# Performance work log

Hardware: AMD Instinct MI355X
Metric: run time of the kernel (lower is better)

## Reference

```python
import jax, jax.numpy as jnp
import numpy as np

NUM_EMBEDDINGS = 2048
EMBEDDING_DIM = 256
COMMITMENT_COST = 0.25


def setup_inputs() -> dict:
    key = jax.random.key(0)
    k1, k2 = jax.random.split(key)
    inputs = jax.random.normal(k1, (2, EMBEDDING_DIM, 24, 24, 24), dtype=jnp.float32)
    embedding_weight = jax.random.normal(k2, (NUM_EMBEDDINGS, EMBEDDING_DIM), dtype=jnp.float32)
    return {"inputs": inputs, "embedding_weight": embedding_weight}


def reference(inputs, embedding_weight):
    # [B, C, D, H, W] -> [B, D, H, W, C]
    x = jnp.transpose(inputs, (0, 2, 3, 4, 1))
    in_shape = x.shape
    flat = x.reshape(-1, EMBEDDING_DIM)  # [N, D]

    distances = (
        jnp.sum(flat * flat, axis=1, keepdims=True)
        + jnp.sum(embedding_weight * embedding_weight, axis=1)
        - 2.0 * flat @ embedding_weight.T
    )
    encoding_indices = jnp.argmin(distances, axis=1)  # [N]
    encodings = jax.nn.one_hot(encoding_indices, NUM_EMBEDDINGS, dtype=jnp.float32)  # [N, K]

    # Gather instead of one_hot @ W (same math, no redundant GEMM)
    quantized = embedding_weight[encoding_indices].reshape(in_shape)

    e_latent_loss = jnp.mean((jax.lax.stop_gradient(quantized) - x) ** 2)
    loss = COMMITMENT_COST * e_latent_loss

    # Straight-through estimator
    quantized_st = x + jax.lax.stop_gradient(quantized - x)

    avg_probs = jnp.mean(encodings, axis=0)
    perplexity = jnp.exp(-jnp.sum(avg_probs * jnp.log(avg_probs + 1e-10)))

    quantized_out = jnp.transpose(quantized_st, (0, 4, 1, 2, 3))
    return (loss, quantized_out, perplexity, encodings, encoding_indices[:, None])
```

## Files before the change

kernel.cpp:

```cpp
#include <hip/hip_runtime.h>

#define S_SP   13824
#define CHAN   256
#define NQ     27648
#define KCODES 2048
#define CS     3538944
#define OFF_Q   1
#define OFF_PPL 7077889
#define OFF_ENC 7077890LL
#define OFF_IDX 63700994LL

typedef __bf16 bf16x8 __attribute__((ext_vector_type(8)));
typedef float  f32x4  __attribute__((ext_vector_type(4)));

#define GLOAD_LDS16(g, s)                                                      \
  __builtin_amdgcn_global_load_lds(                                            \
      (const __attribute__((address_space(1))) void*)(g),                      \
      (__attribute__((address_space(3))) void*)(s), 16, 0, 0)

__device__ __forceinline__ unsigned int f2bf(float f) {
  unsigned int u = __float_as_uint(f);
  unsigned int r = u + 0x7FFFu + ((u >> 16) & 1u);
  return r >> 16;
}
__device__ __forceinline__ float bf2f(unsigned int h) {
  return __uint_as_float(h << 16);
}
__device__ __forceinline__ void fsplit(float f, unsigned int& hi, unsigned int& lo) {
  hi = f2bf(f);
  float r = f - bf2f(hi);
  lo = f2bf(r);
}

__global__ __launch_bounds__(256) void prep_w(const float* __restrict__ W,
                                              unsigned short* __restrict__ Wh,
                                              unsigned short* __restrict__ Wl,
                                              float* __restrict__ wn) {
  int g = blockIdx.x * 256 + threadIdx.x;
  int row = g >> 5;
  int d0 = (g & 31) * 8;
  const float* Wp = W + (size_t)row * CHAN + d0;
  float v[8];
  *(float4*)(v) = *(const float4*)Wp;
  *(float4*)(v + 4) = *(const float4*)(Wp + 4);
  float s = 0.f;
  unsigned int h[8], l[8];
#pragma unroll
  for (int j = 0; j < 8; ++j) {
    s = fmaf(v[j], v[j], s);
    fsplit(v[j], h[j], l[j]);
  }
  int4 ph, pl;
  ph.x = (int)(h[0] | (h[1] << 16)); ph.y = (int)(h[2] | (h[3] << 16));
  ph.z = (int)(h[4] | (h[5] << 16)); ph.w = (int)(h[6] | (h[7] << 16));
  pl.x = (int)(l[0] | (l[1] << 16)); pl.y = (int)(l[2] | (l[3] << 16));
  pl.z = (int)(l[4] | (l[5] << 16)); pl.w = (int)(l[6] | (l[7] << 16));
  *(int4*)(Wh + (size_t)row * CHAN + d0) = ph;
  *(int4*)(Wl + (size_t)row * CHAN + d0) = pl;
  for (int off = 16; off; off >>= 1) s += __shfl_down(s, off);
  if ((threadIdx.x & 31) == 0) wn[row] = s;
}

__global__ __launch_bounds__(256) void prep_x(const float* __restrict__ X,
                                              unsigned short* __restrict__ Xh,
                                              unsigned short* __restrict__ Xl) {
  __shared__ float xs[32 * 257];
  int t = threadIdx.x;
  int qb = blockIdx.x * 32;
  int b = qb / S_SP, s0 = qb % S_SP;
  const float* xp = X + (size_t)b * CS + s0;
  int q = t & 31;
  int db = t >> 5;
  for (int r = 0; r < 32; ++r) {
    int d = db + (r << 3);
    xs[q * 257 + d] = xp[(size_t)d * S_SP + q];
  }
  __syncthreads();
  int row = t >> 3, c8 = t & 7;
  size_t obase = (size_t)(qb + row) * CHAN;
  const float* rp0 = xs + row * 257;
#pragma unroll
  for (int j = 0; j < 4; ++j) {
    int d = j * 64 + c8 * 8;
    const float* rp = rp0 + d;
    unsigned int h[8], l[8];
#pragma unroll
    for (int e = 0; e < 8; ++e) fsplit(rp[e], h[e], l[e]);
    int4 ph, pl;
    ph.x = (int)(h[0] | (h[1] << 16)); ph.y = (int)(h[2] | (h[3] << 16));
    ph.z = (int)(h[4] | (h[5] << 16)); ph.w = (int)(h[6] | (h[7] << 16));
    pl.x = (int)(l[0] | (l[1] << 16)); pl.y = (int)(l[2] | (l[3] << 16));
    pl.z = (int)(l[4] | (l[5] << 16)); pl.w = (int)(l[6] | (l[7] << 16));
    *(int4*)(Xh + obase + d) = ph;
    *(int4*)(Xl + obase + d) = pl;
  }
}

__global__ __launch_bounds__(256, 2) void dist_mfma(const unsigned short* __restrict__ Xh,
                                                    const unsigned short* __restrict__ Xl,
                                                    const unsigned short* __restrict__ Wh,
                                                    const unsigned short* __restrict__ Wl,
                                                    const float* __restrict__ wn,
                                                    float* __restrict__ rB1,
                                                    int* __restrict__ rI1,
                                                    float* __restrict__ rB2) {
  __shared__ __align__(16) unsigned short sW[2][2][4096];
  __shared__ float wnl[1024];
  int t = threadIdx.x;
  int w = t >> 6, l = t & 63;
  int lr = l & 15, lc = l >> 4;
  int kg = blockIdx.x & 1;
  int qb = (blockIdx.x >> 1) * 128;
  int kofs = kg << 10;

  for (int j = t; j < 1024; j += 256) wnl[j] = wn[kofs + j];

  bf16x8 ah[2][8], al[2][8];
#pragma unroll
  for (int s = 0; s < 2; ++s) {
    size_t base = (size_t)(qb + w * 32 + s * 16 + lr) * CHAN + lc * 8;
#pragma unroll
    for (int c = 0; c < 8; ++c) {
      ah[s][c] = *(const bf16x8*)(Xh + base + c * 32);
      al[s][c] = *(const bf16x8*)(Xl + base + c * 32);
    }
  }

  float b1[2][4], b2[2][4]; int i1[2][4];
#pragma unroll
  for (int s = 0; s < 2; ++s)
#pragma unroll
    for (int r = 0; r < 4; ++r) { b1[s][r] = 3.4e38f; b2[s][r] = 3.4e38f; i1[s][r] = 0; }

  auto stage = [&](int buf, int kt) {
    size_t rb = (size_t)(kofs + (kt << 4) + lr) * CHAN + lc * 8;
    GLOAD_LDS16(Wh + rb + w * 32,        &sW[buf][0][w * 512]);
    GLOAD_LDS16(Wh + rb + (w + 4) * 32,  &sW[buf][0][(w + 4) * 512]);
    GLOAD_LDS16(Wl + rb + w * 32,        &sW[buf][1][w * 512]);
    GLOAD_LDS16(Wl + rb + (w + 4) * 32,  &sW[buf][1][(w + 4) * 512]);
  };

  stage(0, 0);
  __syncthreads();

  for (int kt = 0; kt < 64; ++kt) {
    int cur = kt & 1;
    if (kt < 63) stage(cur ^ 1, kt + 1);
    f32x4 a0 = {0.f, 0.f, 0.f, 0.f}, a1 = {0.f, 0.f, 0.f, 0.f};
#pragma unroll
    for (int c = 0; c < 8; ++c) {
      bf16x8 bh = *(const bf16x8*)&sW[cur][0][c * 512 + (l << 3)];
      bf16x8 bl = *(const bf16x8*)&sW[cur][1][c * 512 + (l << 3)];
      a0 = __builtin_amdgcn_mfma_f32_16x16x32_bf16(ah[0][c], bh, a0, 0, 0, 0);
      a1 = __builtin_amdgcn_mfma_f32_16x16x32_bf16(ah[1][c], bh, a1, 0, 0, 0);
      a0 = __builtin_amdgcn_mfma_f32_16x16x32_bf16(al[0][c], bh, a0, 0, 0, 0);
      a1 = __builtin_amdgcn_mfma_f32_16x16x32_bf16(al[1][c], bh, a1, 0, 0, 0);
      a0 = __builtin_amdgcn_mfma_f32_16x16x32_bf16(ah[0][c], bl, a0, 0, 0, 0);
      a1 = __builtin_amdgcn_mfma_f32_16x16x32_bf16(ah[1][c], bl, a1, 0, 0, 0);
    }
    int k = kofs + (kt << 4) + lr;
    float wnk = wnl[(kt << 4) + lr];
#pragma unroll
    for (int r = 0; r < 4; ++r) {
      float s0 = fmaf(-2.0f, a0[r], wnk);
      bool lt0 = s0 < b1[0][r];
      b2[0][r] = fminf(b2[0][r], fmaxf(s0, b1[0][r]));
      b1[0][r] = lt0 ? s0 : b1[0][r];
      i1[0][r] = lt0 ? k : i1[0][r];
      float s1 = fmaf(-2.0f, a1[r], wnk);
      bool lt1 = s1 < b1[1][r];
      b2[1][r] = fminf(b2[1][r], fmaxf(s1, b1[1][r]));
      b1[1][r] = lt1 ? s1 : b1[1][r];
      i1[1][r] = lt1 ? k : i1[1][r];
    }
    __syncthreads();
  }

#pragma unroll
  for (int m = 1; m < 16; m <<= 1) {
#pragma unroll
    for (int s = 0; s < 2; ++s)
#pragma unroll
      for (int r = 0; r < 4; ++r) {
        float ob1 = __shfl_xor(b1[s][r], m);
        int   oi  = __shfl_xor(i1[s][r], m);
        float ob2 = __shfl_xor(b2[s][r], m);
        bool sw = (ob1 < b1[s][r]) || (ob1 == b1[s][r] && oi < i1[s][r]);
        b2[s][r] = fminf(fmaxf(b1[s][r], ob1), fminf(b2[s][r], ob2));
        b1[s][r] = sw ? ob1 : b1[s][r];
        i1[s][r] = sw ? oi : i1[s][r];
      }
  }
  if (lr == 0) {
#pragma unroll
    for (int s = 0; s < 2; ++s)
#pragma unroll
      for (int r = 0; r < 4; ++r) {
        int q = qb + w * 32 + s * 16 + lc * 4 + r;
        size_t o = (size_t)kg * NQ + q;
        rB1[o] = b1[s][r]; rI1[o] = i1[s][r]; rB2[o] = b2[s][r];
      }
  }
}

__global__ __launch_bounds__(256) void merge_emit(const float* __restrict__ rB1,
                                                  const int* __restrict__ rI1,
                                                  const float* __restrict__ rB2,
                                                  float* __restrict__ outF,
                                                  int* __restrict__ flagcount,
                                                  int2* __restrict__ flaglist) {
  int t = threadIdx.x;
  int r = t >> 5, j = t & 31;
  int n = blockIdx.x * 8 + r;

  float B1 = rB1[n]; int I1 = rI1[n]; float B2 = rB2[n];
  float c1 = rB1[NQ + n]; int ci = rI1[NQ + n]; float c2 = rB2[NQ + n];
  bool sw = (c1 < B1) || (c1 == B1 && ci < I1);
  float nb2 = fminf(fmaxf(B1, c1), fminf(B2, c2));
  float nb1 = sw ? c1 : B1;
  int   ni  = sw ? ci : I1;

  if (j == 0) {
    if (nb2 - nb1 < 0.05f) {
      int slot = atomicAdd(flagcount, 1);
      flaglist[slot] = make_int2(n, ni);
    }
    outF[OFF_IDX + n] = (float)ni;
  }

  float* row = outF + OFF_ENC + (size_t)n * KCODES;
#pragma unroll
  for (int k = 0; k < 32; ++k) {
    int col = 2 * j + 64 * k;
    union { float f[2]; unsigned long long u; } v;
    v.f[0] = (col == ni) ? 1.0f : 0.0f;
    v.f[1] = (col + 1 == ni) ? 1.0f : 0.0f;
    __builtin_nontemporal_store(v.u, (unsigned long long*)(row + col));
  }
}

__global__ __launch_bounds__(256) void refine2(const float* __restrict__ X,
                                               const float* __restrict__ W,
                                               const int* __restrict__ flagcount,
                                               const int2* __restrict__ flaglist,
                                               float* __restrict__ outF) {
  __shared__ double xd[CHAN];
  __shared__ double rv[256];
  __shared__ int    ri[256];
  int t = threadIdx.x;
  int cnt = flagcount[0];
  for (int jj = blockIdx.x; jj < cnt; jj += gridDim.x) {
    __syncthreads();
    int2 e = flaglist[jj];
    int n = e.x, prov = e.y;
    int b = n / S_SP, s = n % S_SP;
    xd[t] = (double)X[(size_t)b * CS + (size_t)t * S_SP + s];
    __syncthreads();

    double best = 1e300;
    int bi = 1 << 30;
    for (int j8 = 0; j8 < 8; ++j8) {
      int k = t * 8 + j8;
      const float* Wp = W + (size_t)k * CHAN;
      double dsum = 0.0;
      for (int d = 0; d < CHAN; ++d) {
        double df = xd[d] - (double)Wp[d];
        dsum = fma(df, df, dsum);
      }
      if (dsum < best) { best = dsum; bi = k; }
    }
    rv[t] = best; ri[t] = bi;
    __syncthreads();
    for (int off = 128; off > 0; off >>= 1) {
      if (t < off) {
        if (rv[t + off] < rv[t] || (rv[t + off] == rv[t] && ri[t + off] < ri[t])) {
          rv[t] = rv[t + off]; ri[t] = ri[t + off];
        }
      }
      __syncthreads();
    }
    if (t == 0) {
      int fin = ri[0];
      outF[OFF_IDX + n] = (float)fin;
      if (fin != prov) {
        float* row = outF + OFF_ENC + (size_t)n * KCODES;
        row[prov] = 0.0f;
        row[fin]  = 1.0f;
      }
    }
  }
}

__global__ __launch_bounds__(256) void scatter_stats(const float* __restrict__ X,
                                                     const float* __restrict__ W,
                                                     float* __restrict__ outF,
                                                     int* __restrict__ counts,
                                                     float* __restrict__ loss_acc) {
  __shared__ int sidx[64];
  __shared__ float wred[4];
  int t = threadIdx.x;
  int q = t & 63, cg = t >> 6;
  int n = blockIdx.x * 64 + q;
  if (t < 64) {
    int idx = (int)outF[OFF_IDX + n];
    sidx[t] = idx;
    atomicAdd(&counts[idx], 1);
  }
  __syncthreads();
  int idx = sidx[q];
  int b = n / S_SP, s = n % S_SP;
  const float* Wp = W + (size_t)idx * CHAN;
  const float* xp = X + (size_t)b * CS + s;
  float* qp = outF + OFF_Q + (size_t)b * CS + s;

  float lsum = 0.f;
#pragma unroll 8
  for (int k = 0; k < 64; ++k) {
    int c = cg + (k << 2);
    float wv = Wp[c];
    float xv = xp[(size_t)c * S_SP];
    qp[(size_t)c * S_SP] = wv;
    float df = wv - xv;
    lsum = fmaf(df, df, lsum);
  }

  for (int off = 32; off; off >>= 1) lsum += __shfl_down(lsum, off);
  if ((t & 63) == 0) wred[t >> 6] = lsum;
  __syncthreads();
  if (t == 0) atomicAdd(loss_acc, wred[0] + wred[1] + wred[2] + wred[3]);
}

__global__ __launch_bounds__(256) void finalize(const int* __restrict__ counts,
                                                const float* __restrict__ loss_acc,
                                                float* __restrict__ outF) {
  __shared__ double red[256];
  int t = threadIdx.x;
  double H = 0.0;
  for (int k = t; k < KCODES; k += 256) {
    double p = (double)counts[k] / (double)NQ;
    H += p * log(p + 1e-10);
  }
  red[t] = H;
  __syncthreads();
  for (int off = 128; off > 0; off >>= 1) {
    if (t < off) red[t] += red[t + off];
    __syncthreads();
  }
  if (t == 0) {
    outF[0] = 0.25f * (loss_acc[0] / 7077888.0f);
    outF[OFF_PPL] = (float)exp(-red[0]);
  }
}

extern "C" void kernel_launch(void* const* d_in, const int* in_sizes, int n_in,
                              void* d_out, int out_size, void* d_ws, size_t ws_size,
                              hipStream_t stream) {
  const float* X = (const float*)d_in[0];
  const float* W = (const float*)d_in[1];
  float* outF = (float*)d_out;
  char* ws = (char*)d_ws;
  float* wn        = (float*)ws;
  int*   counts    = (int*)(ws + 8192);
  float* loss_acc  = (float*)(ws + 16384);
  int*   flagcount = (int*)(ws + 16388);
  int2*  flaglist  = (int2*)(ws + 32768);
  float* rB1       = (float*)(ws + 262144);
  int*   rI1       = (int*)(ws + 483328);
  float* rB2       = (float*)(ws + 704512);
  unsigned short* Wh = (unsigned short*)(ws + 1048576);
  unsigned short* Wl = (unsigned short*)(ws + 2097152);
  unsigned short* Xh = (unsigned short*)(ws + 3145728);
  unsigned short* Xl = Xh + (size_t)NQ * CHAN;

  hipMemsetAsync(ws + 8192, 0, 8200, stream);

  prep_w<<<256, 256, 0, stream>>>(W, Wh, Wl, wn);
  prep_x<<<NQ / 32, 256, 0, stream>>>(X, Xh, Xl);
  dist_mfma<<<(NQ / 128) * 2, 256, 0, stream>>>(Xh, Xl, Wh, Wl, wn, rB1, rI1, rB2);
  merge_emit<<<NQ / 8, 256, 0, stream>>>(rB1, rI1, rB2, outF, flagcount, flaglist);
  refine2<<<256, 256, 0, stream>>>(X, W, flagcount, flaglist, outF);
  scatter_stats<<<NQ / 64, 256, 0, stream>>>(X, W, outF, counts, loss_acc);
  finalize<<<1, 256, 0, stream>>>(counts, loss_acc, outF);
}
```

Baseline: 268.5 us.

## Defer one-hot emission to stats kernel, drop memset, double-tile W staging

The one-hot encodings row writes move out of the merge kernel into the final scatter/stats kernel, which now runs after refinement. This removes the refine kernel's patch-up writes and lets merge run one thread per query. The memset is folded into prep_w's first block. The distance kernel now stages two 16-code tiles per barrier to halve the syncs, at the cost of doubled LDS. Quantized output stores become nontemporal.

```diff
diff --git a/kernel.cpp b/kernel.cpp
--- a/kernel.cpp
+++ b/kernel.cpp
@@ -35,7 +35,11 @@
 __global__ __launch_bounds__(256) void prep_w(const float* __restrict__ W,
                                               unsigned short* __restrict__ Wh,
                                               unsigned short* __restrict__ Wl,
-                                              float* __restrict__ wn) {
+                                              float* __restrict__ wn,
+                                              int* __restrict__ zero_base) {
+  if (blockIdx.x == 0) {
+    for (int j = threadIdx.x; j < 2050; j += 256) zero_base[j] = 0;
+  }
   int g = blockIdx.x * 256 + threadIdx.x;
   int row = g >> 5;
   int d0 = (g & 31) * 8;
@@ -104,7 +108,7 @@
                                                     float* __restrict__ rB1,
                                                     int* __restrict__ rI1,
                                                     float* __restrict__ rB2) {
-  __shared__ __align__(16) unsigned short sW[2][2][4096];
+  __shared__ __align__(16) unsigned short sW[2][2][2][4096];
   __shared__ float wnl[1024];
   int t = threadIdx.x;
   int w = t >> 6, l = t & 63;
@@ -132,46 +136,54 @@
 #pragma unroll
     for (int r = 0; r < 4; ++r) { b1[s][r] = 3.4e38f; b2[s][r] = 3.4e38f; i1[s][r] = 0; }
 
-  auto stage = [&](int buf, int kt) {
-    size_t rb = (size_t)(kofs + (kt << 4) + lr) * CHAN + lc * 8;
-    GLOAD_LDS16(Wh + rb + w * 32,        &sW[buf][0][w * 512]);
-    GLOAD_LDS16(Wh + rb + (w + 4) * 32,  &sW[buf][0][(w + 4) * 512]);
-    GLOAD_LDS16(Wl + rb + w * 32,        &sW[buf][1][w * 512]);
-    GLOAD_LDS16(Wl + rb + (w + 4) * 32,  &sW[buf][1][(w + 4) * 512]);
+  auto stage2 = [&](int pp, int it) {
+#pragma unroll
+    for (int sub = 0; sub < 2; ++sub) {
+      int kt = it * 2 + sub;
+      size_t rb = (size_t)(kofs + (kt << 4) + lr) * CHAN + lc * 8;
+      GLOAD_LDS16(Wh + rb + w * 32,       &sW[pp][sub][0][w * 512]);
+      GLOAD_LDS16(Wh + rb + (w + 4) * 32, &sW[pp][sub][0][(w + 4) * 512]);
+      GLOAD_LDS16(Wl + rb + w * 32,       &sW[pp][sub][1][w * 512]);
+      GLOAD_LDS16(Wl + rb + (w + 4) * 32, &sW[pp][sub][1][(w + 4) * 512]);
+    }
   };
 
-  stage(0, 0);
-  __syncthreads();
-
-  for (int kt = 0; kt < 64; ++kt) {
-    int cur = kt & 1;
-    if (kt < 63) stage(cur ^ 1, kt + 1);
-    f32x4 a0 = {0.f, 0.f, 0.f, 0.f}, a1 = {0.f, 0.f, 0.f, 0.f};
-#pragma unroll
-    for (int c = 0; c < 8; ++c) {
-      bf16x8 bh = *(const bf16x8*)&sW[cur][0][c * 512 + (l << 3)];
-      bf16x8 bl = *(const bf16x8*)&sW[cur][1][c * 512 + (l << 3)];
-      a0 = __builtin_amdgcn_mfma_f32_16x16x32_bf16(ah[0][c], bh, a0, 0, 0, 0);
-      a1 = __builtin_amdgcn_mfma_f32_16x16x32_bf16(ah[1][c], bh, a1, 0, 0, 0);
-      a0 = __builtin_amdgcn_mfma_f32_16x16x32_bf16(al[0][c], bh, a0, 0, 0, 0);
-      a1 = __builtin_amdgcn_mfma_f32_16x16x32_bf16(al[1][c], bh, a1, 0, 0, 0);
-      a0 = __builtin_amdgcn_mfma_f32_16x16x32_bf16(ah[0][c], bl, a0, 0, 0, 0);
-      a1 = __builtin_amdgcn_mfma_f32_16x16x32_bf16(ah[1][c], bl, a1, 0, 0, 0);
-    }
-    int k = kofs + (kt << 4) + lr;
-    float wnk = wnl[(kt << 4) + lr];
-#pragma unroll
-    for (int r = 0; r < 4; ++r) {
-      float s0 = fmaf(-2.0f, a0[r], wnk);
-      bool lt0 = s0 < b1[0][r];
-      b2[0][r] = fminf(b2[0][r], fmaxf(s0, b1[0][r]));
-      b1[0][r] = lt0 ? s0 : b1[0][r];
-      i1[0][r] = lt0 ? k : i1[0][r];
-      float s1 = fmaf(-2.0f, a1[r], wnk);
-      bool lt1 = s1 < b1[1][r];
-      b2[1][r] = fminf(b2[1][r], fmaxf(s1, b1[1][r]));
-      b1[1][r] = lt1 ? s1 : b1[1][r];
-      i1[1][r] = lt1 ? k : i1[1][r];
+  stage2(0, 0);
+  __syncthreads();
+
+  for (int it2 = 0; it2 < 32; ++it2) {
+    int p = it2 & 1;
+    if (it2 < 31) stage2(p ^ 1, it2 + 1);
+#pragma unroll
+    for (int sub = 0; sub < 2; ++sub) {
+      int kt = it2 * 2 + sub;
+      f32x4 a0 = {0.f, 0.f, 0.f, 0.f}, a1 = {0.f, 0.f, 0.f, 0.f};
+#pragma unroll
+      for (int c = 0; c < 8; ++c) {
+        bf16x8 bh = *(const bf16x8*)&sW[p][sub][0][c * 512 + (l << 3)];
+        bf16x8 bl = *(const bf16x8*)&sW[p][sub][1][c * 512 + (l << 3)];
+        a0 = __builtin_amdgcn_mfma_f32_16x16x32_bf16(ah[0][c], bh, a0, 0, 0, 0);
+        a1 = __builtin_amdgcn_mfma_f32_16x16x32_bf16(ah[1][c], bh, a1, 0, 0, 0);
+        a0 = __builtin_amdgcn_mfma_f32_16x16x32_bf16(al[0][c], bh, a0, 0, 0, 0);
+        a1 = __builtin_amdgcn_mfma_f32_16x16x32_bf16(al[1][c], bh, a1, 0, 0, 0);
+        a0 = __builtin_amdgcn_mfma_f32_16x16x32_bf16(ah[0][c], bl, a0, 0, 0, 0);
+        a1 = __builtin_amdgcn_mfma_f32_16x16x32_bf16(ah[1][c], bl, a1, 0, 0, 0);
+      }
+      int k = kofs + (kt << 4) + lr;
+      float wnk = wnl[(kt << 4) + lr];
+#pragma unroll
+      for (int r = 0; r < 4; ++r) {
+        float s0 = fmaf(-2.0f, a0[r], wnk);
+        bool lt0 = s0 < b1[0][r];
+        b2[0][r] = fminf(b2[0][r], fmaxf(s0, b1[0][r]));
+        b1[0][r] = lt0 ? s0 : b1[0][r];
+        i1[0][r] = lt0 ? k : i1[0][r];
+        float s1 = fmaf(-2.0f, a1[r], wnk);
+        bool lt1 = s1 < b1[1][r];
+        b2[1][r] = fminf(b2[1][r], fmaxf(s1, b1[1][r]));
+        b1[1][r] = lt1 ? s1 : b1[1][r];
+        i1[1][r] = lt1 ? k : i1[1][r];
+      }
     }
     __syncthreads();
   }
@@ -203,47 +215,31 @@
   }
 }
 
-__global__ __launch_bounds__(256) void merge_emit(const float* __restrict__ rB1,
-                                                  const int* __restrict__ rI1,
-                                                  const float* __restrict__ rB2,
-                                                  float* __restrict__ outF,
-                                                  int* __restrict__ flagcount,
-                                                  int2* __restrict__ flaglist) {
-  int t = threadIdx.x;
-  int r = t >> 5, j = t & 31;
-  int n = blockIdx.x * 8 + r;
-
+__global__ __launch_bounds__(256) void merge_k(const float* __restrict__ rB1,
+                                               const int* __restrict__ rI1,
+                                               const float* __restrict__ rB2,
+                                               float* __restrict__ idx_out,
+                                               int* __restrict__ flagcount,
+                                               int2* __restrict__ flaglist) {
+  int n = blockIdx.x * 256 + threadIdx.x;
   float B1 = rB1[n]; int I1 = rI1[n]; float B2 = rB2[n];
   float c1 = rB1[NQ + n]; int ci = rI1[NQ + n]; float c2 = rB2[NQ + n];
   bool sw = (c1 < B1) || (c1 == B1 && ci < I1);
   float nb2 = fminf(fmaxf(B1, c1), fminf(B2, c2));
   float nb1 = sw ? c1 : B1;
   int   ni  = sw ? ci : I1;
-
-  if (j == 0) {
-    if (nb2 - nb1 < 0.05f) {
-      int slot = atomicAdd(flagcount, 1);
-      flaglist[slot] = make_int2(n, ni);
-    }
-    outF[OFF_IDX + n] = (float)ni;
-  }
-
-  float* row = outF + OFF_ENC + (size_t)n * KCODES;
-#pragma unroll
-  for (int k = 0; k < 32; ++k) {
-    int col = 2 * j + 64 * k;
-    union { float f[2]; unsigned long long u; } v;
-    v.f[0] = (col == ni) ? 1.0f : 0.0f;
-    v.f[1] = (col + 1 == ni) ? 1.0f : 0.0f;
-    __builtin_nontemporal_store(v.u, (unsigned long long*)(row + col));
-  }
+  if (nb2 - nb1 < 0.05f) {
+    int slot = atomicAdd(flagcount, 1);
+    flaglist[slot] = make_int2(n, ni);
+  }
+  idx_out[n] = (float)ni;
 }
 
 __global__ __launch_bounds__(256) void refine2(const float* __restrict__ X,
                                                const float* __restrict__ W,
                                                const int* __restrict__ flagcount,
                                                const int2* __restrict__ flaglist,
-                                               float* __restrict__ outF) {
+                                               float* __restrict__ idx_out) {
   __shared__ double xd[CHAN];
   __shared__ double rv[256];
   __shared__ int    ri[256];
@@ -251,8 +247,7 @@
   int cnt = flagcount[0];
   for (int jj = blockIdx.x; jj < cnt; jj += gridDim.x) {
     __syncthreads();
-    int2 e = flaglist[jj];
-    int n = e.x, prov = e.y;
+    int n = flaglist[jj].x;
     int b = n / S_SP, s = n % S_SP;
     xd[t] = (double)X[(size_t)b * CS + (size_t)t * S_SP + s];
     __syncthreads();
@@ -279,34 +274,47 @@
       }
       __syncthreads();
     }
-    if (t == 0) {
-      int fin = ri[0];
-      outF[OFF_IDX + n] = (float)fin;
-      if (fin != prov) {
-        float* row = outF + OFF_ENC + (size_t)n * KCODES;
-        row[prov] = 0.0f;
-        row[fin]  = 1.0f;
-      }
-    }
-  }
-}
-
-__global__ __launch_bounds__(256) void scatter_stats(const float* __restrict__ X,
-                                                     const float* __restrict__ W,
-                                                     float* __restrict__ outF,
-                                                     int* __restrict__ counts,
-                                                     float* __restrict__ loss_acc) {
+    if (t == 0) idx_out[n] = (float)ri[0];
+  }
+}
+
+__global__ __launch_bounds__(256) void emit_stats(const float* __restrict__ X,
+                                                  const float* __restrict__ W,
+                                                  float* __restrict__ outF,
+                                                  int* __restrict__ counts,
+                                                  float* __restrict__ loss_acc) {
   __shared__ int sidx[64];
   __shared__ float wred[4];
   int t = threadIdx.x;
-  int q = t & 63, cg = t >> 6;
-  int n = blockIdx.x * 64 + q;
+  int qb = blockIdx.x * 64;
   if (t < 64) {
-    int idx = (int)outF[OFF_IDX + n];
+    int idx = (int)outF[OFF_IDX + qb + t];
     sidx[t] = idx;
     atomicAdd(&counts[idx], 1);
   }
   __syncthreads();
+
+  {
+    float* rp = outF + OFF_ENC + (size_t)qb * KCODES + t * 8;
+    for (int q = 0; q < 64; ++q) {
+      int ni = sidx[q];
+      bool own = (ni >> 3) == t;
+      unsigned long long one = (ni & 1) ? 0x3F80000000000000ULL : 0x3F800000ULL;
+      int e2 = (ni >> 1) & 3;
+      unsigned long long v0 = (own && e2 == 0) ? one : 0ULL;
+      unsigned long long v1 = (own && e2 == 1) ? one : 0ULL;
+      unsigned long long v2 = (own && e2 == 2) ? one : 0ULL;
+      unsigned long long v3 = (own && e2 == 3) ? one : 0ULL;
+      __builtin_nontemporal_store(v0, (unsigned long long*)rp);
+      __builtin_nontemporal_store(v1, (unsigned long long*)(rp + 2));
+      __builtin_nontemporal_store(v2, (unsigned long long*)(rp + 4));
+      __builtin_nontemporal_store(v3, (unsigned long long*)(rp + 6));
+      rp += KCODES;
+    }
+  }
+
+  int q = t & 63, cg = t >> 6;
+  int n = qb + q;
   int idx = sidx[q];
   int b = n / S_SP, s = n % S_SP;
   const float* Wp = W + (size_t)idx * CHAN;
@@ -319,7 +327,7 @@
     int c = cg + (k << 2);
     float wv = Wp[c];
     float xv = xp[(size_t)c * S_SP];
-    qp[(size_t)c * S_SP] = wv;
+    __builtin_nontemporal_store(wv, qp + (size_t)c * S_SP);
     float df = wv - xv;
     lsum = fmaf(df, df, lsum);
   }
@@ -372,13 +380,11 @@
   unsigned short* Xh = (unsigned short*)(ws + 3145728);
   unsigned short* Xl = Xh + (size_t)NQ * CHAN;
 
-  hipMemsetAsync(ws + 8192, 0, 8200, stream);
-
-  prep_w<<<256, 256, 0, stream>>>(W, Wh, Wl, wn);
+  prep_w<<<256, 256, 0, stream>>>(W, Wh, Wl, wn, (int*)(ws + 8192));
   prep_x<<<NQ / 32, 256, 0, stream>>>(X, Xh, Xl);
   dist_mfma<<<(NQ / 128) * 2, 256, 0, stream>>>(Xh, Xl, Wh, Wl, wn, rB1, rI1, rB2);
-  merge_emit<<<NQ / 8, 256, 0, stream>>>(rB1, rI1, rB2, outF, flagcount, flaglist);
-  refine2<<<256, 256, 0, stream>>>(X, W, flagcount, flaglist, outF);
-  scatter_stats<<<NQ / 64, 256, 0, stream>>>(X, W, outF, counts, loss_acc);
+  merge_k<<<NQ / 256, 256, 0, stream>>>(rB1, rI1, rB2, outF + OFF_IDX, flagcount, flaglist);
+  refine2<<<256, 256, 0, stream>>>(X, W, flagcount, flaglist, outF + OFF_IDX);
+  emit_stats<<<NQ / 64, 256, 0, stream>>>(X, W, outF, counts, loss_acc);
   finalize<<<1, 256, 0, stream>>>(counts, loss_acc, outF);
 }
```

New measurement: 349.7 us. +30.2%, slower.
